# Optimization experiments

Measured on AMD Instinct MI355X. Metric: run time of the kernel, lower is better.

Reference implementation:

```python
import jax, jax.numpy as jnp
import numpy as np


def setup_inputs() -> dict:
    key = jax.random.key(0)
    k1, k2 = jax.random.split(key)
    B, C, H, W = 8, 64, 64, 64
    x = jax.random.normal(k1, (B, C, H, W), dtype=jnp.float32)
    stdv = 1.0 / np.sqrt(C)
    weight = jax.random.uniform(k2, (C, C), dtype=jnp.float32, minval=-stdv, maxval=stdv)
    return {"x": x, "weight": weight}


def reference(x, weight):
    B, C, H, W = x.shape
    N = H * W
    xf = x.reshape(B, C, N)            # [B, C, N]
    g_x = jnp.transpose(xf, (0, 2, 1))  # [B, N, C] (also theta_x)
    # f[b, i, j] = sum_c x[b, c, i] * x[b, c, j]
    f = jnp.einsum('bic,bcj->bij', g_x, xf)  # [B, N, N]
    adj = jax.nn.softmax(f, axis=-1)
    support = jnp.einsum('bnc,cd->bnd', g_x, weight)  # [B, N, C]
    y = jnp.einsum('bij,bjc->bic', adj, support)      # [B, N, C]
    y = jnp.transpose(y, (0, 2, 1)).reshape(B, C, H, W)
    return y + x
```

## Files before the change

### kernel.cpp

```cpp
#include <hip/hip_runtime.h>
#include <stdint.h>


#define NTOK 4096
#define CCH  64

typedef float v4f __attribute__((ext_vector_type(4)));
typedef __bf16 v8bf __attribute__((ext_vector_type(8)));
typedef unsigned short v8us __attribute__((ext_vector_type(8)));
typedef __fp16 v2fp __attribute__((ext_vector_type(2)));
typedef _Float16 v8h __attribute__((ext_vector_type(8)));

__device__ __forceinline__ unsigned short f2bf(float f) {
    union { float f; unsigned int u; } c; c.f = f;
    unsigned int r = c.u + 0x7fffu + ((c.u >> 16) & 1u);
    return (unsigned short)(r >> 16);
}

__device__ __forceinline__ v8bf ld8(const unsigned short* p) {
    union { v8us s; v8bf b; } u;
    u.s = *(const v8us*)p;
    return u.b;
}

__device__ __forceinline__ unsigned int pkbf(float a, float b) {
    union { float f; unsigned int u; } ua, ub; ua.f = a; ub.f = b;
    return __builtin_amdgcn_perm(ub.u, ua.u, 0x07060302u);
}

__device__ __forceinline__ float ex2(float x) {
#if __has_builtin(__builtin_amdgcn_exp2f)
    return __builtin_amdgcn_exp2f(x);
#else
    return exp2f(x);
#endif
}

__device__ __forceinline__ void gload_lds16(const void* g, void* l) {
    __builtin_amdgcn_global_load_lds(
        (const __attribute__((address_space(1))) unsigned int*)g,
        (__attribute__((address_space(3))) unsigned int*)l,
        16, 0, 0);
}

__global__ __launch_bounds__(256) void prep_kernel(
    const float* __restrict__ x,
    const float* __restrict__ w,
    unsigned short* __restrict__ xT,
    unsigned short* __restrict__ sT)
{
    __shared__ float Xf[64 * 65];

    const int tid  = threadIdx.x;
    const int lane = tid & 63;
    const int wv   = __builtin_amdgcn_readfirstlane(tid >> 6);
    const int b    = blockIdx.x & 7;
    const int n0   = (blockIdx.x >> 3) * 64;

    const float* xb = x + (size_t)b * CCH * NTOK + n0 + lane;
    #pragma unroll
    for (int k = 0; k < 16; ++k) {
        const int c = wv * 16 + k;
        Xf[c * 65 + lane] = xb[(size_t)c * NTOK];
    }
    __syncthreads();

    {
        const int n  = tid >> 2;
        const int c0 = (tid & 3) * 16;
        unsigned int pk[8];
        #pragma unroll
        for (int k = 0; k < 8; ++k) {
            const float a = Xf[(c0 + 2 * k) * 65 + n];
            const float c2 = Xf[(c0 + 2 * k + 1) * 65 + n];
            pk[k] = (unsigned int)f2bf(a) | ((unsigned int)f2bf(c2) << 16);
        }
        unsigned short* xtr = xT + ((size_t)b * NTOK + n0 + n) * CCH + c0;
        *(uint4*)(xtr)     = *(uint4*)(pk);
        *(uint4*)(xtr + 8) = *(uint4*)(pk + 4);
    }

    float acc[16];
    #pragma unroll
    for (int d = 0; d < 16; ++d) acc[d] = 0.f;

    #pragma unroll 4
    for (int c = 0; c < 64; ++c) {
        const float xc = Xf[c * 65 + lane];
        const float* wr = w + c * 64 + wv * 16;
        #pragma unroll
        for (int d = 0; d < 16; ++d) acc[d] = fmaf(xc, wr[d], acc[d]);
    }
    unsigned short* stb = sT + (size_t)b * CCH * NTOK + n0 + lane;
    #pragma unroll
    for (int d = 0; d < 16; ++d)
        stb[(size_t)(wv * 16 + d) * NTOK] = f2bf(acc[d]);
}

__global__ __launch_bounds__(512, 4) void flash_kernel(
    const unsigned short* __restrict__ xT,
    const unsigned short* __restrict__ sT,
    unsigned short* __restrict__ part_o,
    float* __restrict__ part_l,
    int nchunk, int chunk_len)
{
    __shared__ __align__(16) unsigned short Kt[2][64 * 64];
    __shared__ __align__(16) unsigned short Vt[2][64 * 64];

    const int tid  = threadIdx.x;
    const int w    = tid >> 6;
    const int lane = tid & 63;
    const int quad = lane >> 4;
    const int l16  = lane & 15;

    const int L     = blockIdx.x;
    const int b     = L & 7;
    const int t     = L >> 3;
    const int i0    = (t & 15) * 256;
    const int chunk = t >> 4;
    const int irow  = i0 + w * 32;
    const int jb    = chunk * chunk_len;

    const unsigned short* xTb = xT + (size_t)b * NTOK * CCH;
    const unsigned short* sTb = sT + (size_t)b * CCH * NTOK;

    const int srow = w * 8 + (lane >> 3);
    const int sc   = (lane & 7) ^ (lane >> 3);
    const int ksrow = 32 * (srow >> 5) + 8 * ((srow & 12) >> 2)
                    + 4 * ((srow >> 4) & 1) + (srow & 3);

    auto stage = [&](int j0, int bf) {
        gload_lds16(xTb + (size_t)(j0 + ksrow) * CCH + sc * 8, Kt[bf] + w * 512);
        gload_lds16(sTb + (size_t)srow * NTOK + j0 + sc * 8,   Vt[bf] + w * 512);
    };

    stage(jb, 0);

    v8bf aq0[2], aq1[2];
    #pragma unroll
    for (int m = 0; m < 2; ++m) {
        const unsigned short* qr = xTb + (size_t)(irow + m * 16 + l16) * CCH + quad * 8;
        aq0[m] = ld8(qr);
        aq1[m] = ld8(qr + 32);
    }

    const float L2E = 1.4426950408889634f;
    float negm2[2];
    #pragma unroll
    for (int m = 0; m < 2; ++m) {
        float msq = 0.f;
        #pragma unroll
        for (int i = 0; i < 8; ++i) {
            float e0 = (float)aq0[m][i], e1 = (float)aq1[m][i];
            msq = fmaf(e0, e0, msq);
            msq = fmaf(e1, e1, msq);
        }
        msq += __shfl_xor(msq, 16);
        msq += __shfl_xor(msq, 32);
        negm2[m] = -msq * L2E;
    }

    v4f o[2][4];
    #pragma unroll
    for (int m = 0; m < 2; ++m)
        #pragma unroll
        for (int ct = 0; ct < 4; ++ct) { o[m][ct][0]=0.f; o[m][ct][1]=0.f; o[m][ct][2]=0.f; o[m][ct][3]=0.f; }
    float rsum[2] = {0.f, 0.f};

    int cur = 0;
    for (int jj = 0; jj < chunk_len; jj += 64) {
        __syncthreads();
        if (jj + 64 < chunk_len)
            stage(jb + jj + 64, cur ^ 1);

        const unsigned short* Kc = Kt[cur];
        const unsigned short* Vc = Vt[cur];

        #pragma unroll
        for (int h = 0; h < 2; ++h) {
            uint2 pk[2][2];
            #pragma unroll
            for (int jtl = 0; jtl < 2; ++jtl) {
                const int krow = 32 * h + 16 * jtl + l16;
                const unsigned short* kb = Kc + krow * 64;
                const int c0 = quad ^ (krow & 7);
                v8bf bk0 = ld8(kb + c0 * 8);
                v8bf bk1 = ld8(kb + (c0 ^ 4) * 8);
                #pragma unroll
                for (int m = 0; m < 2; ++m) {
                    v4f z; z[0]=0.f; z[1]=0.f; z[2]=0.f; z[3]=0.f;
                    z = __builtin_amdgcn_mfma_f32_16x16x32_bf16(bk0, aq0[m], z, 0, 0, 0);
                    z = __builtin_amdgcn_mfma_f32_16x16x32_bf16(bk1, aq1[m], z, 0, 0, 0);
                    const float p0 = ex2(fmaf(z[0], L2E, negm2[m]));
                    const float p1 = ex2(fmaf(z[1], L2E, negm2[m]));
                    const float p2 = ex2(fmaf(z[2], L2E, negm2[m]));
                    const float p3 = ex2(fmaf(z[3], L2E, negm2[m]));
                    rsum[m] += (p0 + p1) + (p2 + p3);
                    pk[m][jtl].x = pkbf(p0, p1);
                    pk[m][jtl].y = pkbf(p2, p3);
                }
            }

            union { unsigned int u[4]; v8bf b; } pb[2];
            #pragma unroll
            for (int m = 0; m < 2; ++m) {
                pb[m].u[0] = pk[m][0].x; pb[m].u[1] = pk[m][0].y;
                pb[m].u[2] = pk[m][1].x; pb[m].u[3] = pk[m][1].y;
            }

            #pragma unroll
            for (int ct = 0; ct < 4; ++ct) {
                const int vrow = 16 * ct + l16;
                const unsigned short* vb = Vc + vrow * 64;
                const int cc = (4 * h + quad) ^ (vrow & 7);
                v8bf bv = ld8(vb + cc * 8);
                #pragma unroll
                for (int m = 0; m < 2; ++m)
                    o[m][ct] = __builtin_amdgcn_mfma_f32_16x16x32_bf16(bv, pb[m].b, o[m][ct], 0, 0, 0);
            }
        }
        cur ^= 1;
    }

    const size_t pbase = (size_t)(b * nchunk + chunk) * NTOK + irow;
    #pragma unroll
    for (int m = 0; m < 2; ++m) {
        float t2 = rsum[m];
        t2 += __shfl_xor(t2, 16);
        t2 += __shfl_xor(t2, 32);
        if (quad == 0) part_l[pbase + m * 16 + l16] = t2;
    }
    unsigned short* po = part_o + pbase * 64;
    #pragma unroll
    for (int m = 0; m < 2; ++m)
        #pragma unroll
        for (int ct = 0; ct < 4; ++ct) {
            union { struct { v2fp a, b; } h; uint2 u; } cv;
            cv.h.a = __builtin_amdgcn_cvt_pkrtz(o[m][ct][0], o[m][ct][1]);
            cv.h.b = __builtin_amdgcn_cvt_pkrtz(o[m][ct][2], o[m][ct][3]);
            *(uint2*)(po + (size_t)(m * 16 + l16) * 64 + ct * 16 + quad * 4) = cv.u;
        }
}

__global__ __launch_bounds__(256) void combine_kernel(
    const unsigned short* __restrict__ part_o,
    const float* __restrict__ part_l,
    const float* __restrict__ x,
    float* __restrict__ out,
    int nchunk)
{
    __shared__ float Of[64 * 65];
    const int tid = threadIdx.x;
    const int b  = blockIdx.x & 7;
    const int i0 = (blockIdx.x >> 3) * 64;
    const int row = tid >> 2;
    const int seg = tid & 3;

    float acc[16];
    #pragma unroll
    for (int k = 0; k < 16; ++k) acc[k] = 0.f;
    float lt = 0.f;

    auto body = [&](int ch) {
        const size_t base = (size_t)(b * nchunk + ch) * NTOK + i0 + row;
        lt += part_l[base];
        const unsigned short* po = part_o + base * 64 + seg * 16;
        v8h a = *(const v8h*)(po);
        v8h c2 = *(const v8h*)(po + 8);
        #pragma unroll
        for (int k = 0; k < 8; ++k) {
            acc[k]     += (float)a[k];
            acc[8 + k] += (float)c2[k];
        }
    };
    if (nchunk == 4) { body(0); body(1); body(2); body(3); }
    else { for (int ch = 0; ch < nchunk; ++ch) body(ch); }

    const float inv = 1.f / lt;
    #pragma unroll
    for (int k = 0; k < 16; ++k) Of[row * 65 + seg * 16 + k] = acc[k] * inv;
    __syncthreads();

    const int c    = tid >> 2;
    const int part = tid & 3;
    const float* xrow = x   + ((size_t)b * CCH + c) * NTOK + i0 + part * 16;
    float*       orow = out + ((size_t)b * CCH + c) * NTOK + i0 + part * 16;
    #pragma unroll
    for (int i4 = 0; i4 < 4; ++i4) {
        float4 xv = *(const float4*)(xrow + i4 * 4);
        float4 ov;
        ov.x = Of[(part * 16 + i4 * 4 + 0) * 65 + c] + xv.x;
        ov.y = Of[(part * 16 + i4 * 4 + 1) * 65 + c] + xv.y;
        ov.z = Of[(part * 16 + i4 * 4 + 2) * 65 + c] + xv.z;
        ov.w = Of[(part * 16 + i4 * 4 + 3) * 65 + c] + xv.w;
        *(float4*)(orow + i4 * 4) = ov;
    }
}

extern "C" void kernel_launch(void* const* d_in, const int* in_sizes, int n_in,
                              void* d_out, int out_size, void* d_ws, size_t ws_size,
                              hipStream_t stream) {
    const float* x = (const float*)d_in[0];
    const float* w = (const float*)d_in[1];
    float* out = (float*)d_out;

    const size_t xT_elems = (size_t)8 * NTOK * CCH;
    unsigned short* xT = (unsigned short*)d_ws;
    unsigned short* sT = xT + xT_elems;
    char* rest = (char*)d_ws + 2 * xT_elems * sizeof(unsigned short);

    int KS = 4;
    while (KS > 1) {
        size_t need = 2 * xT_elems * sizeof(unsigned short)
                    + (size_t)KS * ((size_t)8 * NTOK * CCH * 2 + (size_t)8 * NTOK * 4);
        if (need <= ws_size) break;
        KS >>= 1;
    }
    unsigned short* part_o = (unsigned short*)rest;
    float* part_l = (float*)(rest + (size_t)KS * 8 * NTOK * CCH * 2);

    prep_kernel<<<512, 256, 0, stream>>>(x, w, xT, sT);
    flash_kernel<<<128 * KS, 512, 0, stream>>>(xT, sT, part_o, part_l, KS, NTOK / KS);
    combine_kernel<<<512, 256, 0, stream>>>(part_o, part_l, x, out, KS);
}
```

Measured before the change: 122.5 us.

## Software-pipeline PV matmul one tile behind QK and coalesce support stores

The flash kernel now computes the softmax probabilities for the current key tile, then runs the P·V MFMAs for the previous tile. It uses a third V buffer in LDS so the exp/convert work can overlap with the matrix ops. Separately, the support-projection kernel stages its results through shared memory so it can write bf16 output as 16-byte vector stores instead of scattered 2-byte stores. The cost is more LDS use (an extra 8KB V buffer), extra registers for the carried probabilities, and additional barriers in the projection kernel.

```diff
diff --git a/kernel.cpp b/kernel.cpp
--- a/kernel.cpp
+++ b/kernel.cpp
@@ -91,10 +91,26 @@
         #pragma unroll
         for (int d = 0; d < 16; ++d) acc[d] = fmaf(xc, wr[d], acc[d]);
     }
-    unsigned short* stb = sT + (size_t)b * CCH * NTOK + n0 + lane;
+
+    __syncthreads();
     #pragma unroll
     for (int d = 0; d < 16; ++d)
-        stb[(size_t)(wv * 16 + d) * NTOK] = f2bf(acc[d]);
+        Xf[(wv * 16 + d) * 65 + lane] = acc[d];
+    __syncthreads();
+    {
+        const int d   = tid >> 2;
+        const int prt = tid & 3;
+        const float* src = Xf + d * 65 + prt * 16;
+        unsigned int pk2[8];
+        #pragma unroll
+        for (int k = 0; k < 8; ++k)
+            pk2[k] = (unsigned int)f2bf(src[2 * k])
+                   | ((unsigned int)f2bf(src[2 * k + 1]) << 16);
+        unsigned short* dst = sT + (size_t)b * CCH * NTOK
+                            + (size_t)d * NTOK + n0 + prt * 16;
+        *(uint4*)(dst)     = *(uint4*)(pk2);
+        *(uint4*)(dst + 8) = *(uint4*)(pk2 + 4);
+    }
 }
 
 __global__ __launch_bounds__(512, 4) void flash_kernel(
@@ -105,7 +121,7 @@
     int nchunk, int chunk_len)
 {
     __shared__ __align__(16) unsigned short Kt[2][64 * 64];
-    __shared__ __align__(16) unsigned short Vt[2][64 * 64];
+    __shared__ __align__(16) unsigned short Vt[3][64 * 64];
 
     const int tid  = threadIdx.x;
     const int w    = tid >> 6;
@@ -129,12 +145,19 @@
     const int ksrow = 32 * (srow >> 5) + 8 * ((srow & 12) >> 2)
                     + 4 * ((srow >> 4) & 1) + (srow & 3);
 
-    auto stage = [&](int j0, int bf) {
-        gload_lds16(xTb + (size_t)(j0 + ksrow) * CCH + sc * 8, Kt[bf] + w * 512);
-        gload_lds16(sTb + (size_t)srow * NTOK + j0 + sc * 8,   Vt[bf] + w * 512);
+    auto stageK = [&](int j0, unsigned short* kd) {
+        gload_lds16(xTb + (size_t)(j0 + ksrow) * CCH + sc * 8, kd + w * 512);
     };
-
-    stage(jb, 0);
+    auto stageV = [&](int j0, unsigned short* vd) {
+        gload_lds16(sTb + (size_t)srow * NTOK + j0 + sc * 8, vd + w * 512);
+    };
+
+    unsigned short* vcur  = Vt[0];
+    unsigned short* vnext = Vt[1];
+    unsigned short* vprev = Vt[2];
+
+    stageK(jb, Kt[0]);
+    stageV(jb, vcur);
 
     v8bf aq0[2], aq1[2];
     #pragma unroll
@@ -167,18 +190,45 @@
         for (int ct = 0; ct < 4; ++ct) { o[m][ct][0]=0.f; o[m][ct][1]=0.f; o[m][ct][2]=0.f; o[m][ct][3]=0.f; }
     float rsum[2] = {0.f, 0.f};
 
+    uint2 pkp[2][4];
+
+    auto pvStep = [&](const unsigned short* Vb) {
+        #pragma unroll
+        for (int h = 0; h < 2; ++h) {
+            union { unsigned int u[4]; v8bf bv8; } pb[2];
+            #pragma unroll
+            for (int m = 0; m < 2; ++m) {
+                pb[m].u[0] = pkp[m][2 * h].x;
+                pb[m].u[1] = pkp[m][2 * h].y;
+                pb[m].u[2] = pkp[m][2 * h + 1].x;
+                pb[m].u[3] = pkp[m][2 * h + 1].y;
+            }
+            #pragma unroll
+            for (int ct = 0; ct < 4; ++ct) {
+                const int vrow = 16 * ct + l16;
+                const unsigned short* vb = Vb + vrow * 64;
+                const int cc = (4 * h + quad) ^ (vrow & 7);
+                v8bf bv = ld8(vb + cc * 8);
+                #pragma unroll
+                for (int m = 0; m < 2; ++m)
+                    o[m][ct] = __builtin_amdgcn_mfma_f32_16x16x32_bf16(bv, pb[m].bv8, o[m][ct], 0, 0, 0);
+            }
+        }
+    };
+
     int cur = 0;
     for (int jj = 0; jj < chunk_len; jj += 64) {
         __syncthreads();
-        if (jj + 64 < chunk_len)
-            stage(jb + jj + 64, cur ^ 1);
+        if (jj + 64 < chunk_len) {
+            stageK(jb + jj + 64, Kt[cur ^ 1]);
+            stageV(jb + jj + 64, vnext);
+        }
 
         const unsigned short* Kc = Kt[cur];
-        const unsigned short* Vc = Vt[cur];
-
+
+        uint2 pkn[2][4];
         #pragma unroll
         for (int h = 0; h < 2; ++h) {
-            uint2 pk[2][2];
             #pragma unroll
             for (int jtl = 0; jtl < 2; ++jtl) {
                 const int krow = 32 * h + 16 * jtl + l16;
@@ -196,31 +246,24 @@
                     const float p2 = ex2(fmaf(z[2], L2E, negm2[m]));
                     const float p3 = ex2(fmaf(z[3], L2E, negm2[m]));
                     rsum[m] += (p0 + p1) + (p2 + p3);
-                    pk[m][jtl].x = pkbf(p0, p1);
-                    pk[m][jtl].y = pkbf(p2, p3);
+                    pkn[m][2 * h + jtl].x = pkbf(p0, p1);
+                    pkn[m][2 * h + jtl].y = pkbf(p2, p3);
                 }
             }
-
-            union { unsigned int u[4]; v8bf b; } pb[2];
+        }
+
+        if (jj > 0)
+            pvStep(vprev);
+
+        #pragma unroll
+        for (int m = 0; m < 2; ++m)
             #pragma unroll
-            for (int m = 0; m < 2; ++m) {
-                pb[m].u[0] = pk[m][0].x; pb[m].u[1] = pk[m][0].y;
-                pb[m].u[2] = pk[m][1].x; pb[m].u[3] = pk[m][1].y;
-            }
-
-            #pragma unroll
-            for (int ct = 0; ct < 4; ++ct) {
-                const int vrow = 16 * ct + l16;
-                const unsigned short* vb = Vc + vrow * 64;
-                const int cc = (4 * h + quad) ^ (vrow & 7);
-                v8bf bv = ld8(vb + cc * 8);
-                #pragma unroll
-                for (int m = 0; m < 2; ++m)
-                    o[m][ct] = __builtin_amdgcn_mfma_f32_16x16x32_bf16(bv, pb[m].b, o[m][ct], 0, 0, 0);
-            }
-        }
+            for (int i = 0; i < 4; ++i) pkp[m][i] = pkn[m][i];
+
+        unsigned short* tp = vprev; vprev = vcur; vcur = vnext; vnext = tp;
         cur ^= 1;
     }
+    pvStep(vprev);
 
     const size_t pbase = (size_t)(b * nchunk + chunk) * NTOK + irow;
     #pragma unroll
```

Result: slower. 125.1 us (+2.1%).

## Load K/V fragments directly from global into registers, drop LDS staging

Applied to the files above, without the earlier changes.

The flash kernel no longer stages K and V tiles through double-buffered LDS with global_load_lds. Each wave now reads its MFMA operand fragments straight from global memory via pointer walks and relies on the cache, which removes the per-iteration barriers. The token ordering for K is permuted so it matches the MFMA layout. Blocks shrink from 512 to 256 threads with twice as many blocks. The prep kernel also transposes the support output through LDS so the sT stores become coalesced 16-byte writes. The risk is redundant global and L2 traffic, since several waves now load the same K/V data without sharing it.

```diff
diff --git a/kernel.cpp b/kernel.cpp
--- a/kernel.cpp
+++ b/kernel.cpp
@@ -34,13 +34,6 @@
 #else
     return exp2f(x);
 #endif
-}
-
-__device__ __forceinline__ void gload_lds16(const void* g, void* l) {
-    __builtin_amdgcn_global_load_lds(
-        (const __attribute__((address_space(1))) unsigned int*)g,
-        (__attribute__((address_space(3))) unsigned int*)l,
-        16, 0, 0);
 }
 
 __global__ __launch_bounds__(256) void prep_kernel(
@@ -91,22 +84,35 @@
         #pragma unroll
         for (int d = 0; d < 16; ++d) acc[d] = fmaf(xc, wr[d], acc[d]);
     }
-    unsigned short* stb = sT + (size_t)b * CCH * NTOK + n0 + lane;
+
+    __syncthreads();
     #pragma unroll
     for (int d = 0; d < 16; ++d)
-        stb[(size_t)(wv * 16 + d) * NTOK] = f2bf(acc[d]);
-}
-
-__global__ __launch_bounds__(512, 4) void flash_kernel(
+        Xf[(wv * 16 + d) * 65 + lane] = acc[d];
+    __syncthreads();
+    {
+        const int d   = tid >> 2;
+        const int prt = tid & 3;
+        const float* src = Xf + d * 65 + prt * 16;
+        unsigned int pk2[8];
+        #pragma unroll
+        for (int k = 0; k < 8; ++k)
+            pk2[k] = (unsigned int)f2bf(src[2 * k])
+                   | ((unsigned int)f2bf(src[2 * k + 1]) << 16);
+        unsigned short* dst = sT + (size_t)b * CCH * NTOK
+                            + (size_t)d * NTOK + n0 + prt * 16;
+        *(uint4*)(dst)     = *(uint4*)(pk2);
+        *(uint4*)(dst + 8) = *(uint4*)(pk2 + 4);
+    }
+}
+
+__global__ __launch_bounds__(256, 4) void flash_kernel(
     const unsigned short* __restrict__ xT,
     const unsigned short* __restrict__ sT,
     unsigned short* __restrict__ part_o,
     float* __restrict__ part_l,
     int nchunk, int chunk_len)
 {
-    __shared__ __align__(16) unsigned short Kt[2][64 * 64];
-    __shared__ __align__(16) unsigned short Vt[2][64 * 64];
-
     const int tid  = threadIdx.x;
     const int w    = tid >> 6;
     const int lane = tid & 63;
@@ -116,25 +122,26 @@
     const int L     = blockIdx.x;
     const int b     = L & 7;
     const int t     = L >> 3;
-    const int i0    = (t & 15) * 256;
-    const int chunk = t >> 4;
+    const int i0    = (t & 31) * 128;
+    const int chunk = t >> 5;
     const int irow  = i0 + w * 32;
     const int jb    = chunk * chunk_len;
 
     const unsigned short* xTb = xT + (size_t)b * NTOK * CCH;
     const unsigned short* sTb = sT + (size_t)b * CCH * NTOK;
 
-    const int srow = w * 8 + (lane >> 3);
-    const int sc   = (lane & 7) ^ (lane >> 3);
-    const int ksrow = 32 * (srow >> 5) + 8 * ((srow & 12) >> 2)
-                    + 4 * ((srow >> 4) & 1) + (srow & 3);
-
-    auto stage = [&](int j0, int bf) {
-        gload_lds16(xTb + (size_t)(j0 + ksrow) * CCH + sc * 8, Kt[bf] + w * 512);
-        gload_lds16(sTb + (size_t)srow * NTOK + j0 + sc * 8,   Vt[bf] + w * 512);
-    };
-
-    stage(jb, 0);
+    const unsigned short* kp[2][2];
+    #pragma unroll
+    for (int h = 0; h < 2; ++h)
+        #pragma unroll
+        for (int jtl = 0; jtl < 2; ++jtl) {
+            const int tok = 32 * h + 8 * (l16 >> 2) + 4 * jtl + (l16 & 3);
+            kp[h][jtl] = xTb + (size_t)(jb + tok) * CCH + quad * 8;
+        }
+    const unsigned short* vp[4];
+    #pragma unroll
+    for (int ct = 0; ct < 4; ++ct)
+        vp[ct] = sTb + (size_t)(16 * ct + l16) * NTOK + jb + quad * 8;
 
     v8bf aq0[2], aq1[2];
     #pragma unroll
@@ -167,30 +174,33 @@
         for (int ct = 0; ct < 4; ++ct) { o[m][ct][0]=0.f; o[m][ct][1]=0.f; o[m][ct][2]=0.f; o[m][ct][3]=0.f; }
     float rsum[2] = {0.f, 0.f};
 
-    int cur = 0;
+    #pragma unroll 2
     for (int jj = 0; jj < chunk_len; jj += 64) {
-        __syncthreads();
-        if (jj + 64 < chunk_len)
-            stage(jb + jj + 64, cur ^ 1);
-
-        const unsigned short* Kc = Kt[cur];
-        const unsigned short* Vc = Vt[cur];
+        v8bf bk[2][2][2];
+        #pragma unroll
+        for (int h = 0; h < 2; ++h)
+            #pragma unroll
+            for (int jtl = 0; jtl < 2; ++jtl) {
+                bk[h][jtl][0] = ld8(kp[h][jtl]);
+                bk[h][jtl][1] = ld8(kp[h][jtl] + 32);
+            }
+        v8bf bv[4][2];
+        #pragma unroll
+        for (int ct = 0; ct < 4; ++ct) {
+            bv[ct][0] = ld8(vp[ct]);
+            bv[ct][1] = ld8(vp[ct] + 32);
+        }
 
         #pragma unroll
         for (int h = 0; h < 2; ++h) {
             uint2 pk[2][2];
             #pragma unroll
             for (int jtl = 0; jtl < 2; ++jtl) {
-                const int krow = 32 * h + 16 * jtl + l16;
-                const unsigned short* kb = Kc + krow * 64;
-                const int c0 = quad ^ (krow & 7);
-                v8bf bk0 = ld8(kb + c0 * 8);
-                v8bf bk1 = ld8(kb + (c0 ^ 4) * 8);
                 #pragma unroll
                 for (int m = 0; m < 2; ++m) {
                     v4f z; z[0]=0.f; z[1]=0.f; z[2]=0.f; z[3]=0.f;
-                    z = __builtin_amdgcn_mfma_f32_16x16x32_bf16(bk0, aq0[m], z, 0, 0, 0);
-                    z = __builtin_amdgcn_mfma_f32_16x16x32_bf16(bk1, aq1[m], z, 0, 0, 0);
+                    z = __builtin_amdgcn_mfma_f32_16x16x32_bf16(bk[h][jtl][0], aq0[m], z, 0, 0, 0);
+                    z = __builtin_amdgcn_mfma_f32_16x16x32_bf16(bk[h][jtl][1], aq1[m], z, 0, 0, 0);
                     const float p0 = ex2(fmaf(z[0], L2E, negm2[m]));
                     const float p1 = ex2(fmaf(z[1], L2E, negm2[m]));
                     const float p2 = ex2(fmaf(z[2], L2E, negm2[m]));
@@ -201,7 +211,7 @@
                 }
             }
 
-            union { unsigned int u[4]; v8bf b; } pb[2];
+            union { unsigned int u[4]; v8bf bv8; } pb[2];
             #pragma unroll
             for (int m = 0; m < 2; ++m) {
                 pb[m].u[0] = pk[m][0].x; pb[m].u[1] = pk[m][0].y;
@@ -209,17 +219,18 @@
             }
 
             #pragma unroll
-            for (int ct = 0; ct < 4; ++ct) {
-                const int vrow = 16 * ct + l16;
-                const unsigned short* vb = Vc + vrow * 64;
-                const int cc = (4 * h + quad) ^ (vrow & 7);
-                v8bf bv = ld8(vb + cc * 8);
+            for (int ct = 0; ct < 4; ++ct)
                 #pragma unroll
                 for (int m = 0; m < 2; ++m)
-                    o[m][ct] = __builtin_amdgcn_mfma_f32_16x16x32_bf16(bv, pb[m].b, o[m][ct], 0, 0, 0);
-            }
-        }
-        cur ^= 1;
+                    o[m][ct] = __builtin_amdgcn_mfma_f32_16x16x32_bf16(bv[ct][h], pb[m].bv8, o[m][ct], 0, 0, 0);
+        }
+
+        #pragma unroll
+        for (int h = 0; h < 2; ++h)
+            #pragma unroll
+            for (int jtl = 0; jtl < 2; ++jtl) kp[h][jtl] += 64 * CCH;
+        #pragma unroll
+        for (int ct = 0; ct < 4; ++ct) vp[ct] += 64;
     }
 
     const size_t pbase = (size_t)(b * nchunk + chunk) * NTOK + irow;
@@ -320,6 +331,6 @@
     float* part_l = (float*)(rest + (size_t)KS * 8 * NTOK * CCH * 2);
 
     prep_kernel<<<512, 256, 0, stream>>>(x, w, xT, sT);
-    flash_kernel<<<128 * KS, 512, 0, stream>>>(xT, sT, part_o, part_l, KS, NTOK / KS);
+    flash_kernel<<<256 * KS, 256, 0, stream>>>(xT, sT, part_o, part_l, KS, NTOK / KS);
     combine_kernel<<<512, 256, 0, stream>>>(part_o, part_l, x, out, KS);
 }
```

Result: slower. 202.7 us (+65.5%).
